# Optimization experiments

Measured on AMD Instinct MI355X. Metric: run time of the kernel, lower is better.

Reference implementation:

```python
import jax, jax.numpy as jnp
import numpy as np

H, W = 200, 200            # image_size
X_RANGE = (0.0, 100.0)
Y_RANGE = (0.0, 100.0)
SIZE = 36                   # kernel 'size' from source
SIGMA = 3.0
K = SIZE + 1                # kernel is 37x37 (arange(-18, 19))


def _gaussian_kernel():
    r = jnp.arange(-(SIZE // 2), SIZE // 2 + 1, dtype=jnp.float32)
    k1 = jnp.exp(-(r ** 2) / (2.0 * SIGMA ** 2))
    k2 = k1[:, None] * k1[None, :]
    return k2 / k2.sum()    # [K, K]


def setup_inputs() -> dict:
    key = jax.random.key(0)
    # trajectory coords in world units [0, 100) -> spread over whole map
    x_t = jax.random.uniform(key, (512, 64, 2), dtype=jnp.float32) * 100.0
    return {"x_t": x_t}


def reference(x_t):
    B, T, _ = x_t.shape
    x_scale = W / (X_RANGE[1] - X_RANGE[0])
    y_scale = H / (Y_RANGE[1] - Y_RANGE[0])
    # .long() in torch truncates toward zero; inputs are >= 0 here so astype(int32) matches
    x_pix = ((x_t[:, :, 0] - X_RANGE[0]) * x_scale).astype(jnp.int32)   # [B, T]
    y_pix = H - ((x_t[:, :, 1] - Y_RANGE[0]) * y_scale).astype(jnp.int32)
    valid = ~(jnp.isnan(x_t[:, :, 0]) | jnp.isnan(x_t[:, :, 1]))        # [B, T]

    half = SIZE // 2
    x_start = jnp.clip(x_pix - half, 0, W - SIZE)
    y_start = jnp.clip(y_pix - half, 0, H - SIZE)
    x_end = jnp.clip(x_pix + half, 0, W)
    y_end = jnp.clip(y_pix + half, 0, H)
    kx = x_end - x_start    # patch width  (<= 36, kernel[:,:kx] = top-left slice)
    ky = y_end - y_start    # patch height

    kern = _gaussian_kernel()                       # [K, K]
    r = jnp.arange(K)
    c = jnp.arange(K)
    # mask: kernel[:ky, :kx] slice, and point validity            [B, T, K, K]
    mask = ((r[None, None, :, None] < ky[..., None, None])
            & (c[None, None, None, :] < kx[..., None, None])
            & valid[..., None, None])
    vals = jnp.where(mask, kern[None, None, :, :], 0.0)            # [B, T, K, K]
    rows = jnp.clip(y_start[..., None, None] + r[None, None, :, None], 0, H - 1)
    cols = jnp.clip(x_start[..., None, None] + c[None, None, None, :], 0, W - 1)
    rows = jnp.broadcast_to(rows, (B, T, K, K))
    cols = jnp.broadcast_to(cols, (B, T, K, K))
    flat = (rows * W + cols).reshape(B, -1)                        # [B, T*K*K]

    # parallel scatter-add splat of all Gaussian patches
    heat = jnp.zeros((B, H * W), jnp.float32)
    heat = heat.at[jnp.arange(B)[:, None], flat].add(vals.reshape(B, -1))
    heat = heat.reshape(B, H, W)

    # per-image max normalization (max over dim1 then dim2 == max over both)
    m = heat.max(axis=(1, 2), keepdims=True)
    return heat / (m + 1e-10)
```

## Files before the change

### kernel.cpp

```cpp
#include <hip/hip_runtime.h>


#define NT 64
#define TDIM 224
#define NTL 7
#define BLK 512

typedef short bf16x8 __attribute__((ext_vector_type(8)));
typedef float f32x16 __attribute__((ext_vector_type(16)));

static __device__ inline unsigned short f2bf(float f) {
    unsigned int u = __float_as_uint(f);
    u = (u + 0x7FFFu + ((u >> 16) & 1u)) >> 16;
    return (unsigned short)u;
}

struct __align__(16) SMem {
    unsigned short Rm[TDIM][64];
    unsigned short Cm[TDIM][64];
    float k1f[37];
    float wmax[NTL];
};

__global__ __launch_bounds__(BLK) void heatmap_kernel(const float* __restrict__ x_t,
                                                      float* __restrict__ out) {
    __shared__ SMem s;
    const int tid  = threadIdx.x;
    const int lane = tid & 63;
    const int wv   = tid >> 6;
    const int b    = blockIdx.x;

    {
        uint4 z = {0u, 0u, 0u, 0u};
        uint4* base = (uint4*)s.Rm;
        #pragma unroll
        for (int i = 0; i < 7; ++i) base[tid + BLK * i] = z;
    }
    if (tid < 37) {
        float sum = 0.0f, mine = 0.0f;
        #pragma unroll
        for (int i = 0; i < 37; ++i) {
            float r = (float)(i - 18);
            float v = expf(-(r * r) * (1.0f / 18.0f));
            sum += v;
            if (i == tid) mine = v;
        }
        s.k1f[tid] = mine / sum;
    }
    __syncthreads();

    {
        const int p   = (tid >> 2) & 63;
        const int isC = tid >> 8;
        const int j   = tid & 3;
        const float2 xy = *(const float2*)(x_t + (size_t)b * 128 + 2 * p);
        const bool valid = (xy.x == xy.x) && (xy.y == xy.y);
        const int xp = (int)(xy.x * 2.0f);
        const int yp = 200 - (int)(xy.y * 2.0f);
        const int xs = min(max(xp - 18, 0), 164);
        const int ys = min(max(yp - 18, 0), 164);
        const int kx = valid ? (min(max(xp + 18, 0), 200) - xs) : 0;
        const int ky = valid ? (min(max(yp + 18, 0), 200) - ys) : 0;
        const int start = isC ? xs : ys;
        const int len   = isC ? kx : ky;
        char* dst = isC ? (char*)s.Cm : (char*)s.Rm;
        #pragma unroll
        for (int i = 0; i < 9; ++i) {
            const int rel = j * 9 + i;
            if (rel < len) {
                const int row = start + rel;
                const int off = (2 * p) ^ ((row & 7) << 4);
                *(unsigned short*)(dst + row * 128 + off) = f2bf(s.k1f[rel]);
            }
        }
    }
    __syncthreads();

    const int swl = (lane & 7) << 4;

    bf16x8 A[4];
    if (wv < NTL) {
        const char* ab = (const char*)s.Rm + (wv * 32 + (lane & 31)) * 128;
        #pragma unroll
        for (int m = 0; m < 4; ++m)
            A[m] = *(const bf16x8*)(ab + ((16 * (2 * m + (lane >> 5))) ^ swl));
    }

    float gmax = 0.0f;
    if (wv < NTL) {
        for (int tx = 0; tx < NTL; ++tx) {
            const char* bb = (const char*)s.Cm + (tx * 32 + (lane & 31)) * 128;
            f32x16 acc;
            #pragma unroll
            for (int r = 0; r < 16; ++r) acc[r] = 0.0f;
            #pragma unroll
            for (int m = 0; m < 4; ++m) {
                bf16x8 B = *(const bf16x8*)(bb + ((16 * (2 * m + (lane >> 5))) ^ swl));
                acc = __builtin_amdgcn_mfma_f32_32x32x16_bf16(A[m], B, acc, 0, 0, 0);
            }
            #pragma unroll
            for (int r = 0; r < 16; ++r) gmax = fmaxf(gmax, acc[r]);
        }
    }
    #pragma unroll
    for (int off = 32; off > 0; off >>= 1) gmax = fmaxf(gmax, __shfl_xor(gmax, off));
    if (wv < NTL && lane == 0) s.wmax[wv] = gmax;
    __syncthreads();
    float mm = s.wmax[0];
    #pragma unroll
    for (int w = 1; w < NTL; ++w) mm = fmaxf(mm, s.wmax[w]);
    const float scale = 1.0f / (mm + 1e-10f);

    if (wv < NTL) {
        float* ob = out + (size_t)b * (200 * 200);
        const int colbase = lane & 31;
        const int rowoff  = wv * 32 + 4 * (lane >> 5);
        for (int tx = 0; tx < NTL; ++tx) {
            const char* bb = (const char*)s.Cm + (tx * 32 + (lane & 31)) * 128;
            f32x16 acc;
            #pragma unroll
            for (int r = 0; r < 16; ++r) acc[r] = 0.0f;
            #pragma unroll
            for (int m = 0; m < 4; ++m) {
                bf16x8 B = *(const bf16x8*)(bb + ((16 * (2 * m + (lane >> 5))) ^ swl));
                acc = __builtin_amdgcn_mfma_f32_32x32x16_bf16(A[m], B, acc, 0, 0, 0);
            }
            const int gcol = tx * 32 + colbase;
            #pragma unroll
            for (int r = 0; r < 16; ++r) {
                int grow = rowoff + (r & 3) + 8 * (r >> 2);
                if (grow < 200 && gcol < 200)
                    ob[grow * 200 + gcol] = acc[r] * scale;
            }
        }
    }
}

extern "C" void kernel_launch(void* const* d_in, const int* in_sizes, int n_in,
                              void* d_out, int out_size, void* d_ws, size_t ws_size,
                              hipStream_t stream) {
    const float* x_t = (const float*)d_in[0];
    float* out = (float*)d_out;
    const int B = in_sizes[0] / (NT * 2);
    heatmap_kernel<<<B, BLK, 0, stream>>>(x_t, out);
}
```

Baseline: 24.26 us.

## Recompute output with 16x16 MFMA tiles spread over all eight waves

The output pass now uses 16x16x32 bf16 MFMA tiles over 13 row strips and 14 column tiles, where before it used 32x32 tiles on only seven waves. This lets the eighth wave share the store-heavy epilogue and cuts padded work beyond 200 rows and columns. Stores for a row now come in 16-wide runs, so each is less wide, and the launch bound asks for 4 waves per SIMD, which may limit registers.

```diff
diff --git a/kernel.cpp b/kernel.cpp
--- a/kernel.cpp
+++ b/kernel.cpp
@@ -8,6 +8,7 @@
 
 typedef short bf16x8 __attribute__((ext_vector_type(8)));
 typedef float f32x16 __attribute__((ext_vector_type(16)));
+typedef float f32x4  __attribute__((ext_vector_type(4)));
 
 static __device__ inline unsigned short f2bf(float f) {
     unsigned int u = __float_as_uint(f);
@@ -22,8 +23,8 @@
     float wmax[NTL];
 };
 
-__global__ __launch_bounds__(BLK) void heatmap_kernel(const float* __restrict__ x_t,
-                                                      float* __restrict__ out) {
+__global__ __launch_bounds__(BLK, 4) void heatmap_kernel(const float* __restrict__ x_t,
+                                                         float* __restrict__ out) {
     __shared__ SMem s;
     const int tid  = threadIdx.x;
     const int lane = tid & 63;
@@ -78,16 +79,13 @@
 
     const int swl = (lane & 7) << 4;
 
-    bf16x8 A[4];
+    float gmax = 0.0f;
     if (wv < NTL) {
+        bf16x8 A[4];
         const char* ab = (const char*)s.Rm + (wv * 32 + (lane & 31)) * 128;
         #pragma unroll
         for (int m = 0; m < 4; ++m)
             A[m] = *(const bf16x8*)(ab + ((16 * (2 * m + (lane >> 5))) ^ swl));
-    }
-
-    float gmax = 0.0f;
-    if (wv < NTL) {
         for (int tx = 0; tx < NTL; ++tx) {
             const char* bb = (const char*)s.Cm + (tx * 32 + (lane & 31)) * 128;
             f32x16 acc;
@@ -111,26 +109,49 @@
     for (int w = 1; w < NTL; ++w) mm = fmaxf(mm, s.wmax[w]);
     const float scale = 1.0f / (mm + 1e-10f);
 
-    if (wv < NTL) {
+    {
         float* ob = out + (size_t)b * (200 * 200);
-        const int colbase = lane & 31;
-        const int rowoff  = wv * 32 + 4 * (lane >> 5);
-        for (int tx = 0; tx < NTL; ++tx) {
-            const char* bb = (const char*)s.Cm + (tx * 32 + (lane & 31)) * 128;
-            f32x16 acc;
+        for (int sid = wv; sid < 13; sid += 8) {
+            const int r0 = 16 * sid;
+            bf16x8 Af2[2];
+            {
+                const char* ab = (const char*)s.Rm + (r0 + (lane & 15)) * 128;
+                #pragma unroll
+                for (int kk = 0; kk < 2; ++kk)
+                    Af2[kk] = *(const bf16x8*)(ab + ((16 * (lane >> 4) + 64 * kk) ^ swl));
+            }
             #pragma unroll
-            for (int r = 0; r < 16; ++r) acc[r] = 0.0f;
-            #pragma unroll
-            for (int m = 0; m < 4; ++m) {
-                bf16x8 B = *(const bf16x8*)(bb + ((16 * (2 * m + (lane >> 5))) ^ swl));
-                acc = __builtin_amdgcn_mfma_f32_32x32x16_bf16(A[m], B, acc, 0, 0, 0);
-            }
-            const int gcol = tx * 32 + colbase;
-            #pragma unroll
-            for (int r = 0; r < 16; ++r) {
-                int grow = rowoff + (r & 3) + 8 * (r >> 2);
-                if (grow < 200 && gcol < 200)
-                    ob[grow * 200 + gcol] = acc[r] * scale;
+            for (int h2 = 0; h2 < 2; ++h2) {
+                f32x4 acc2[7];
+                #pragma unroll
+                for (int t = 0; t < 7; ++t) {
+                    acc2[t][0] = 0.0f; acc2[t][1] = 0.0f;
+                    acc2[t][2] = 0.0f; acc2[t][3] = 0.0f;
+                }
+                #pragma unroll
+                for (int t = 0; t < 7; ++t) {
+                    const int xt = 7 * h2 + t;
+                    const char* bb = (const char*)s.Cm + (xt * 16 + (lane & 15)) * 128;
+                    #pragma unroll
+                    for (int kk = 0; kk < 2; ++kk) {
+                        bf16x8 Bf = *(const bf16x8*)(bb + ((16 * (lane >> 4) + 64 * kk) ^ swl));
+                        acc2[t] = __builtin_amdgcn_mfma_f32_16x16x32_bf16(Af2[kk], Bf,
+                                                                          acc2[t], 0, 0, 0);
+                    }
+                }
+                const int rl = 4 * (lane >> 4);
+                #pragma unroll
+                for (int j = 0; j < 4; ++j) {
+                    const int grow = r0 + rl + j;
+                    if (grow < 200) {
+                        #pragma unroll
+                        for (int t = 0; t < 7; ++t) {
+                            const int gcol = (7 * h2 + t) * 16 + (lane & 15);
+                            if (gcol < 200)
+                                ob[(size_t)grow * 200 + gcol] = acc2[t][j] * scale;
+                        }
+                    }
+                }
             }
         }
     }
```

Result: slower. 34.48 us (+42.1%).

## Stage heatmap tile in LDS as bf16 and write output with coalesced vector stores

Applied to the files above, without the earlier changes.

Instead of recomputing the rank-1 MFMA products in a second pass after the max reduction, each wave writes its results into a 200x200 bf16 staging buffer in shared memory during the max pass. After the block-wide max, all 8 waves read the staged tile with 16-byte loads, scale it, and write the output with contiguous float4 stores. This removes the duplicate MFMA work and makes global writes fully coalesced. In exchange, LDS use grows to about 137 KB, which limits each CU to one block, and outputs are rounded to bf16 before scaling, which adds precision error.

```diff
diff --git a/kernel.cpp b/kernel.cpp
--- a/kernel.cpp
+++ b/kernel.cpp
@@ -18,6 +18,7 @@
 struct __align__(16) SMem {
     unsigned short Rm[TDIM][64];
     unsigned short Cm[TDIM][64];
+    unsigned short stage[200][200];
     float k1f[37];
     float wmax[NTL];
 };
@@ -78,16 +79,16 @@
 
     const int swl = (lane & 7) << 4;
 
-    bf16x8 A[4];
+    float gmax = 0.0f;
     if (wv < NTL) {
+        bf16x8 A[4];
         const char* ab = (const char*)s.Rm + (wv * 32 + (lane & 31)) * 128;
         #pragma unroll
         for (int m = 0; m < 4; ++m)
             A[m] = *(const bf16x8*)(ab + ((16 * (2 * m + (lane >> 5))) ^ swl));
-    }
 
-    float gmax = 0.0f;
-    if (wv < NTL) {
+        const int gcolbase = lane & 31;
+        const int rowoff   = wv * 32 + 4 * (lane >> 5);
         for (int tx = 0; tx < NTL; ++tx) {
             const char* bb = (const char*)s.Cm + (tx * 32 + (lane & 31)) * 128;
             f32x16 acc;
@@ -98,8 +99,14 @@
                 bf16x8 B = *(const bf16x8*)(bb + ((16 * (2 * m + (lane >> 5))) ^ swl));
                 acc = __builtin_amdgcn_mfma_f32_32x32x16_bf16(A[m], B, acc, 0, 0, 0);
             }
+            const int gcol = tx * 32 + gcolbase;
             #pragma unroll
-            for (int r = 0; r < 16; ++r) gmax = fmaxf(gmax, acc[r]);
+            for (int r = 0; r < 16; ++r) {
+                const int grow = rowoff + (r & 3) + 8 * (r >> 2);
+                gmax = fmaxf(gmax, acc[r]);
+                if (grow < 200 && gcol < 200)
+                    s.stage[grow][gcol] = f2bf(acc[r]);
+            }
         }
     }
     #pragma unroll
@@ -111,27 +118,22 @@
     for (int w = 1; w < NTL; ++w) mm = fmaxf(mm, s.wmax[w]);
     const float scale = 1.0f / (mm + 1e-10f);
 
-    if (wv < NTL) {
+    {
+        const unsigned short* sp = &s.stage[0][0];
         float* ob = out + (size_t)b * (200 * 200);
-        const int colbase = lane & 31;
-        const int rowoff  = wv * 32 + 4 * (lane >> 5);
-        for (int tx = 0; tx < NTL; ++tx) {
-            const char* bb = (const char*)s.Cm + (tx * 32 + (lane & 31)) * 128;
-            f32x16 acc;
-            #pragma unroll
-            for (int r = 0; r < 16; ++r) acc[r] = 0.0f;
-            #pragma unroll
-            for (int m = 0; m < 4; ++m) {
-                bf16x8 B = *(const bf16x8*)(bb + ((16 * (2 * m + (lane >> 5))) ^ swl));
-                acc = __builtin_amdgcn_mfma_f32_32x32x16_bf16(A[m], B, acc, 0, 0, 0);
-            }
-            const int gcol = tx * 32 + colbase;
-            #pragma unroll
-            for (int r = 0; r < 16; ++r) {
-                int grow = rowoff + (r & 3) + 8 * (r >> 2);
-                if (grow < 200 && gcol < 200)
-                    ob[grow * 200 + gcol] = acc[r] * scale;
-            }
+        for (int i = tid; i < 5000; i += BLK) {
+            uint4 v = *(const uint4*)(sp + 8 * i);
+            float4 lo, hi;
+            lo.x = __uint_as_float(v.x << 16) * scale;
+            lo.y = __uint_as_float(v.x & 0xFFFF0000u) * scale;
+            lo.z = __uint_as_float(v.y << 16) * scale;
+            lo.w = __uint_as_float(v.y & 0xFFFF0000u) * scale;
+            hi.x = __uint_as_float(v.z << 16) * scale;
+            hi.y = __uint_as_float(v.z & 0xFFFF0000u) * scale;
+            hi.z = __uint_as_float(v.w << 16) * scale;
+            hi.w = __uint_as_float(v.w & 0xFFFF0000u) * scale;
+            *(float4*)(ob + 8 * i)     = lo;
+            *(float4*)(ob + 8 * i + 4) = hi;
         }
     }
 }
```

After: 31.91 us. +31.5%, slower.
